# Kernel optimization log

Hardware: AMD Instinct MI355X
Metric: run time of the kernel (lower is better)

The kernel has to match this reference:

```python
import jax, jax.numpy as jnp
import numpy as np

E, N = 8192, 2048
D_EDGE, D_NODE, EMBED, HEADS = 64, 128, 32, 4


def setup_inputs() -> dict:
    key = jax.random.key(0)
    ks = jax.random.split(key, 12)
    s = 0.02
    edge_adj = jax.random.randint(ks[10], (E, E), 0, 2) > 0
    edge_adj = edge_adj | jnp.eye(E, dtype=bool)  # every edge attends to itself
    return {
        "edge_feats": jax.random.normal(ks[0], (E, D_EDGE), jnp.float32),
        "node_feats": jax.random.normal(ks[1], (N, D_NODE), jnp.float32),
        "Wn": s * jax.random.normal(ks[2], (D_NODE, D_EDGE), jnp.float32),
        "Wq": s * jax.random.normal(ks[3], (D_EDGE, D_EDGE), jnp.float32),
        "Wk": s * jax.random.normal(ks[4], (D_EDGE, D_EDGE), jnp.float32),
        "Wv": s * jax.random.normal(ks[5], (D_EDGE, D_EDGE), jnp.float32),
        "Wo": s * jax.random.normal(ks[6], (D_EDGE, D_EDGE), jnp.float32),
        "W1": s * jax.random.normal(ks[7], (D_EDGE, EMBED), jnp.float32),
        "b1": jnp.zeros((EMBED,), jnp.float32),
        "W2": s * jax.random.normal(ks[8], (EMBED, EMBED), jnp.float32),
        "b2": jnp.zeros((EMBED,), jnp.float32),
        "edge_index": jax.random.randint(ks[9], (2, E), 0, N, jnp.int32),
        "edge_adj": edge_adj,
    }


def reference(edge_feats, node_feats, Wn, Wq, Wk, Wv, Wo, W1, b1, W2, b2,
              edge_index, edge_adj):
    # --- EdgeAttention: enrich edges with endpoint node feats (irregular gather) ---
    src, dst = edge_index[0], edge_index[1]
    h = edge_feats + (node_feats[src] + node_feats[dst]) @ Wn  # [E, d_edge]
    hd = D_EDGE // HEADS
    q = (h @ Wq).reshape(E, HEADS, hd)
    k = (h @ Wk).reshape(E, HEADS, hd)
    v = (h @ Wv).reshape(E, HEADS, hd)
    scores = jnp.einsum("qhd,khd->hqk", q, k) / jnp.sqrt(jnp.float32(hd))
    scores = jnp.where(edge_adj[None, :, :], scores, jnp.float32(-1e9))
    attn = jax.nn.softmax(scores, axis=-1)                      # [H, E, E]
    ctx = jnp.einsum("hqk,khd->qhd", attn, v).reshape(E, D_EDGE)
    edge_out = ctx @ Wo                                          # [E, d_edge]
    # --- project: Linear -> GELU -> Linear ---
    x = jax.nn.gelu(edge_out @ W1 + b1)
    return x @ W2 + b2                                           # [E, embed_dim]
```

## Files before the change

kernel.cpp:

```cpp
#include <hip/hip_runtime.h>
#include <hip/hip_bf16.h>
#include <math.h>

#define E_N    8192
#define N_N    2048
#define D_EDGE 64
#define D_NODE 128
#define EMBED  32
#define HEADS  4
#define HD     16

typedef short bf16x8 __attribute__((ext_vector_type(8)));
typedef float f32x4  __attribute__((ext_vector_type(4)));
typedef float f32x16 __attribute__((ext_vector_type(16)));

__global__ __launch_bounds__(256) void prep_kernel(
    const float* __restrict__ edge_feats,
    const float* __restrict__ node_feats,
    const float* __restrict__ Wn,
    const float* __restrict__ Wq,
    const float* __restrict__ Wk,
    const float* __restrict__ Wv,
    const int*   __restrict__ edge_index,
    __hip_bfloat16* __restrict__ Qb,
    __hip_bfloat16* __restrict__ Kb,
    __hip_bfloat16* __restrict__ Vt,
    float* __restrict__ zero_base)
{
    {
        const int gtid = blockIdx.x * 256 + threadIdx.x;
        float4* z = (float4*)zero_base;
        const int nvec = (E_N * D_EDGE + E_N * HEADS) / 4;
        for (int i = gtid; i < nvec; i += 512 * 256)
            z[i] = make_float4(0.f, 0.f, 0.f, 0.f);
    }

    __shared__ float sL[4][D_NODE];
    __shared__ float hL[4][D_EDGE];
    const int lane = threadIdx.x & 63;
    const int es   = threadIdx.x >> 6;
    const int e_base = blockIdx.x * 16;

    for (int it = 0; it < 4; ++it) {
        const int e   = e_base + it * 4 + es;
        const int src = edge_index[e];
        const int dst = edge_index[E_N + e];

        sL[es][lane]      = node_feats[src * D_NODE + lane]
                          + node_feats[dst * D_NODE + lane];
        sL[es][lane + 64] = node_feats[src * D_NODE + 64 + lane]
                          + node_feats[dst * D_NODE + 64 + lane];
        __syncthreads();

        float h = edge_feats[e * D_EDGE + lane];
        #pragma unroll 16
        for (int i = 0; i < D_NODE; ++i)
            h = fmaf(sL[es][i], Wn[i * D_EDGE + lane], h);
        hL[es][lane] = h;
        __syncthreads();

        float q = 0.f, k = 0.f, v = 0.f;
        #pragma unroll 16
        for (int i = 0; i < D_EDGE; ++i) {
            const float hv = hL[es][i];
            q = fmaf(hv, Wq[i * D_EDGE + lane], q);
            k = fmaf(hv, Wk[i * D_EDGE + lane], k);
            v = fmaf(hv, Wv[i * D_EDGE + lane], v);
        }
        Qb[e * D_EDGE + lane] = __float2bfloat16(q * 0.25f);
        Kb[e * D_EDGE + lane] = __float2bfloat16(k);
        Vt[(size_t)lane * E_N + e] = __float2bfloat16(v);
        __syncthreads();
    }
}

__global__ __launch_bounds__(256) void attn_kernel(
    const __hip_bfloat16* __restrict__ Qb,
    const __hip_bfloat16* __restrict__ Kb,
    const __hip_bfloat16* __restrict__ Vt,
    const int* __restrict__ adj,
    float* __restrict__ O_acc,
    float* __restrict__ l_acc)
{
    __shared__ __hip_bfloat16 pS[4][32][40];

    const int tid  = threadIdx.x;
    const int wave = tid >> 6;
    const int lane = tid & 63;
    const int head = wave;
    const int qt = blockIdx.x >> 2;
    const int kq = blockIdx.x & 3;
    const int q0 = qt * 32;
    const int key_base = kq * 2048;
    const int col = lane & 31;

    const bf16x8 qf = *(const bf16x8*)(Qb + (size_t)(q0 + col) * D_EDGE
                                          + head * HD + ((lane >> 5) * 8));

    int moff[16];
    #pragma unroll
    for (int r = 0; r < 16; ++r) {
        const int row = (r & 3) + 8 * (r >> 2) + 4 * (lane >> 5);
        moff[r] = (q0 + row) * E_N + key_base + col;
    }

    const __hip_bfloat16* kptr = Kb + (size_t)(key_base + col) * D_EDGE
                                    + head * HD + ((lane >> 5) * 8);
    const __hip_bfloat16* vptr = Vt + (size_t)(head * HD + (lane & 15)) * E_N
                                    + key_base + ((lane >> 4) * 8);

    f32x4 acc0 = {0.f, 0.f, 0.f, 0.f};
    f32x4 acc1 = {0.f, 0.f, 0.f, 0.f};
    float l16[16];
    #pragma unroll
    for (int r = 0; r < 16; ++r) l16[r] = 0.f;

    __hip_bfloat16* pw = &pS[wave][4 * (lane >> 5)][col];
    const __hip_bfloat16* pA0 = &pS[wave][lane & 15][(lane >> 4) * 8];
    const __hip_bfloat16* pA1 = &pS[wave][16 + (lane & 15)][(lane >> 4) * 8];

    const f32x16 zero16 = {0.f,0.f,0.f,0.f, 0.f,0.f,0.f,0.f,
                           0.f,0.f,0.f,0.f, 0.f,0.f,0.f,0.f};

    for (int c = 0; c < 64; ++c) {
        int mw[16];
        #pragma unroll
        for (int r = 0; r < 16; ++r) mw[r] = adj[moff[r] + c * 32];

        const bf16x8 kf = *(const bf16x8*)(kptr + (size_t)c * 32 * D_EDGE);
        const bf16x8 vf = *(const bf16x8*)(vptr + c * 32);

        f32x16 S = __builtin_amdgcn_mfma_f32_32x32x16_bf16(qf, kf, zero16, 0, 0, 0);

        #pragma unroll
        for (int r = 0; r < 16; ++r) {
            const float p = mw[r] ? __expf(S[r]) : 0.f;
            l16[r] += p;
            pw[((r & 3) + 8 * (r >> 2)) * 40] = __float2bfloat16(p);
        }
        const bf16x8 a0 = *(const bf16x8*)pA0;
        const bf16x8 a1 = *(const bf16x8*)pA1;
        acc0 = __builtin_amdgcn_mfma_f32_16x16x32_bf16(a0, vf, acc0, 0, 0, 0);
        acc1 = __builtin_amdgcn_mfma_f32_16x16x32_bf16(a1, vf, acc1, 0, 0, 0);
    }

    #pragma unroll
    for (int r = 0; r < 16; ++r) {
        float s = l16[r];
        s += __shfl_xor(s, 1);  s += __shfl_xor(s, 2);  s += __shfl_xor(s, 4);
        s += __shfl_xor(s, 8);  s += __shfl_xor(s, 16);
        l16[r] = s;
    }
    if (col == 0) {
        #pragma unroll
        for (int r = 0; r < 16; ++r) {
            const int row = (r & 3) + 8 * (r >> 2) + 4 * (lane >> 5);
            atomicAdd(&l_acc[(q0 + row) * HEADS + head], l16[r]);
        }
    }

    #pragma unroll
    for (int r = 0; r < 4; ++r) {
        const int q  = (lane >> 4) * 4 + r;
        const int d  = head * HD + (lane & 15);
        atomicAdd(&O_acc[(size_t)(q0 + q) * D_EDGE + d],      acc0[r]);
        atomicAdd(&O_acc[(size_t)(q0 + 16 + q) * D_EDGE + d], acc1[r]);
    }
}

__global__ __launch_bounds__(256) void epilogue_kernel(
    const float* __restrict__ O_acc,
    const float* __restrict__ l_acc,
    const float* __restrict__ Wo,
    const float* __restrict__ W1,
    const float* __restrict__ b1,
    const float* __restrict__ W2,
    const float* __restrict__ b2,
    float* __restrict__ out)
{
    __shared__ float ctxS[16][D_EDGE];
    __shared__ float eoS[16][D_EDGE];
    __shared__ float xS[16][EMBED];
    const int tid = threadIdx.x;
    const int e0  = blockIdx.x * 16;

    {
        const int e = tid >> 4, d0 = (tid & 15) * 4;
        const float4 o = *(const float4*)(O_acc + (size_t)(e0 + e) * D_EDGE + d0);
        const float inv = 1.f / l_acc[(e0 + e) * HEADS + (d0 >> 4)];
        ctxS[e][d0]     = o.x * inv;
        ctxS[e][d0 + 1] = o.y * inv;
        ctxS[e][d0 + 2] = o.z * inv;
        ctxS[e][d0 + 3] = o.w * inv;
    }
    __syncthreads();

    for (int o = tid; o < 16 * D_EDGE; o += 256) {
        const int e = o >> 6, d = o & 63;
        float acc = 0.f;
        #pragma unroll 16
        for (int i = 0; i < D_EDGE; ++i)
            acc = fmaf(ctxS[e][i], Wo[i * D_EDGE + d], acc);
        eoS[e][d] = acc;
    }
    __syncthreads();

    for (int o = tid; o < 16 * EMBED; o += 256) {
        const int e = o >> 5, j = o & 31;
        float u = b1[j];
        #pragma unroll 16
        for (int i = 0; i < D_EDGE; ++i)
            u = fmaf(eoS[e][i], W1[i * EMBED + j], u);
        const float t = tanhf(0.7978845608028654f * (u + 0.044715f * u * u * u));
        xS[e][j] = 0.5f * u * (1.f + t);
    }
    __syncthreads();

    for (int o = tid; o < 16 * EMBED; o += 256) {
        const int e = o >> 5, j = o & 31;
        float v = b2[j];
        #pragma unroll
        for (int i = 0; i < EMBED; ++i)
            v = fmaf(xS[e][i], W2[i * EMBED + j], v);
        out[(size_t)(e0 + e) * EMBED + j] = v;
    }
}

extern "C" void kernel_launch(void* const* d_in, const int* in_sizes, int n_in,
                              void* d_out, int out_size, void* d_ws, size_t ws_size,
                              hipStream_t stream)
{
    (void)in_sizes; (void)n_in; (void)out_size; (void)ws_size;
    const float* edge_feats = (const float*)d_in[0];
    const float* node_feats = (const float*)d_in[1];
    const float* Wn = (const float*)d_in[2];
    const float* Wq = (const float*)d_in[3];
    const float* Wk = (const float*)d_in[4];
    const float* Wv = (const float*)d_in[5];
    const float* Wo = (const float*)d_in[6];
    const float* W1 = (const float*)d_in[7];
    const float* b1 = (const float*)d_in[8];
    const float* W2 = (const float*)d_in[9];
    const float* b2 = (const float*)d_in[10];
    const int*   edge_index = (const int*)d_in[11];
    const int*   adj = (const int*)d_in[12];

    __hip_bfloat16* Qb = (__hip_bfloat16*)d_ws;
    __hip_bfloat16* Kb = Qb + (size_t)E_N * D_EDGE;
    __hip_bfloat16* Vt = Kb + (size_t)E_N * D_EDGE;
    float* O_acc = (float*)(Vt + (size_t)E_N * D_EDGE);
    float* l_acc = O_acc + (size_t)E_N * D_EDGE;

    prep_kernel<<<E_N / 16, 256, 0, stream>>>(edge_feats, node_feats,
                                              Wn, Wq, Wk, Wv, edge_index,
                                              Qb, Kb, Vt, O_acc);
    attn_kernel<<<(E_N / 32) * 4, 256, 0, stream>>>(Qb, Kb, Vt, adj,
                                                    O_acc, l_acc);
    epilogue_kernel<<<E_N / 16, 256, 0, stream>>>(O_acc, l_acc,
                                                  Wo, W1, b1, W2, b2,
                                                  (float*)d_out);
}
```

Measured before the change: 524.0 us.

## Pack adjacency mask to bits once, transpose score MFMA, split keys eight ways

Adds a pre-pass that packs the int32 adjacency matrix into a bitmask, so the attention kernel reads 32x fewer mask bytes instead of re-reading the int mask once per head wave. The score MFMA now computes S transposed, which lets each lane own one query row: it writes probabilities as packed bf16 vectors and keeps a single row-sum, so the shuffle reductions go away. The key range is split into eight chunks instead of four, doubling the block count at the cost of more atomic traffic. The pack kernel still reads the full 256 MB int mask once, so total traffic only drops by the removed per-head re-reads.

```diff
diff --git a/kernel.cpp b/kernel.cpp
--- a/kernel.cpp
+++ b/kernel.cpp
@@ -9,6 +9,8 @@
 #define EMBED  32
 #define HEADS  4
 #define HD     16
+#define WPB    256
+#define PPAD   36
 
 typedef short bf16x8 __attribute__((ext_vector_type(8)));
 typedef float f32x4  __attribute__((ext_vector_type(4)));
@@ -74,95 +76,114 @@
     }
 }
 
+__global__ __launch_bounds__(256) void mask_pack_kernel(
+    const int* __restrict__ adj, unsigned int* __restrict__ adjb)
+{
+    const size_t t = (size_t)blockIdx.x * 256 + threadIdx.x;
+    const int4* src = (const int4*)(adj + t * 64);
+    unsigned int w0 = 0, w1 = 0;
+    #pragma unroll
+    for (int j = 0; j < 8; ++j) {
+        const int4 a = src[j];
+        w0 |= (unsigned)(a.x != 0) << (4 * j)
+            | (unsigned)(a.y != 0) << (4 * j + 1)
+            | (unsigned)(a.z != 0) << (4 * j + 2)
+            | (unsigned)(a.w != 0) << (4 * j + 3);
+    }
+    #pragma unroll
+    for (int j = 0; j < 8; ++j) {
+        const int4 a = src[8 + j];
+        w1 |= (unsigned)(a.x != 0) << (4 * j)
+            | (unsigned)(a.y != 0) << (4 * j + 1)
+            | (unsigned)(a.z != 0) << (4 * j + 2)
+            | (unsigned)(a.w != 0) << (4 * j + 3);
+    }
+    ((uint2*)adjb)[t] = make_uint2(w0, w1);
+}
+
 __global__ __launch_bounds__(256) void attn_kernel(
     const __hip_bfloat16* __restrict__ Qb,
     const __hip_bfloat16* __restrict__ Kb,
     const __hip_bfloat16* __restrict__ Vt,
-    const int* __restrict__ adj,
+    const unsigned int* __restrict__ adjb,
     float* __restrict__ O_acc,
     float* __restrict__ l_acc)
 {
-    __shared__ __hip_bfloat16 pS[4][32][40];
+    __shared__ __hip_bfloat16 pS[4][32][PPAD];
 
     const int tid  = threadIdx.x;
     const int wave = tid >> 6;
     const int lane = tid & 63;
     const int head = wave;
-    const int qt = blockIdx.x >> 2;
-    const int kq = blockIdx.x & 3;
+    const int qt = blockIdx.x >> 3;
+    const int kq = blockIdx.x & 7;
     const int q0 = qt * 32;
-    const int key_base = kq * 2048;
+    const int key_base = kq * 1024;
     const int col = lane & 31;
+    const int hh  = lane >> 5;
 
     const bf16x8 qf = *(const bf16x8*)(Qb + (size_t)(q0 + col) * D_EDGE
-                                          + head * HD + ((lane >> 5) * 8));
-
-    int moff[16];
-    #pragma unroll
-    for (int r = 0; r < 16; ++r) {
-        const int row = (r & 3) + 8 * (r >> 2) + 4 * (lane >> 5);
-        moff[r] = (q0 + row) * E_N + key_base + col;
-    }
-
+                                          + head * HD + hh * 8);
     const __hip_bfloat16* kptr = Kb + (size_t)(key_base + col) * D_EDGE
-                                    + head * HD + ((lane >> 5) * 8);
+                                    + head * HD + hh * 8;
     const __hip_bfloat16* vptr = Vt + (size_t)(head * HD + (lane & 15)) * E_N
                                     + key_base + ((lane >> 4) * 8);
+    const unsigned int* mrow = adjb + (size_t)(q0 + col) * WPB + kq * 32;
 
     f32x4 acc0 = {0.f, 0.f, 0.f, 0.f};
     f32x4 acc1 = {0.f, 0.f, 0.f, 0.f};
-    float l16[16];
-    #pragma unroll
-    for (int r = 0; r < 16; ++r) l16[r] = 0.f;
-
-    __hip_bfloat16* pw = &pS[wave][4 * (lane >> 5)][col];
+    float lp = 0.f;
+
+    __hip_bfloat16* pwr = &pS[wave][col][4 * hh];
     const __hip_bfloat16* pA0 = &pS[wave][lane & 15][(lane >> 4) * 8];
-    const __hip_bfloat16* pA1 = &pS[wave][16 + (lane & 15)][(lane >> 4) * 8];
-
-    const f32x16 zero16 = {0.f,0.f,0.f,0.f, 0.f,0.f,0.f,0.f,
-                           0.f,0.f,0.f,0.f, 0.f,0.f,0.f,0.f};
-
-    for (int c = 0; c < 64; ++c) {
-        int mw[16];
+    const __hip_bfloat16* pA1 = pA0 + 16 * PPAD;
+
+    const f32x16 z16 = {0.f,0.f,0.f,0.f, 0.f,0.f,0.f,0.f,
+                        0.f,0.f,0.f,0.f, 0.f,0.f,0.f,0.f};
+
+    for (int cw = 0; cw < 8; ++cw) {
+        const uint4 mv = *(const uint4*)(mrow + cw * 4);
         #pragma unroll
-        for (int r = 0; r < 16; ++r) mw[r] = adj[moff[r] + c * 32];
-
-        const bf16x8 kf = *(const bf16x8*)(kptr + (size_t)c * 32 * D_EDGE);
-        const bf16x8 vf = *(const bf16x8*)(vptr + c * 32);
-
-        f32x16 S = __builtin_amdgcn_mfma_f32_32x32x16_bf16(qf, kf, zero16, 0, 0, 0);
-
-        #pragma unroll
-        for (int r = 0; r < 16; ++r) {
-            const float p = mw[r] ? __expf(S[r]) : 0.f;
-            l16[r] += p;
-            pw[((r & 3) + 8 * (r >> 2)) * 40] = __float2bfloat16(p);
+        for (int cc = 0; cc < 4; ++cc) {
+            const int c = cw * 4 + cc;
+            const unsigned int w =
+                ((cc == 0) ? mv.x : (cc == 1) ? mv.y : (cc == 2) ? mv.z : mv.w)
+                >> (4 * hh);
+
+            const bf16x8 kf = *(const bf16x8*)(kptr + (size_t)c * 32 * D_EDGE);
+            const bf16x8 vf = *(const bf16x8*)(vptr + c * 32);
+
+            const f32x16 S = __builtin_amdgcn_mfma_f32_32x32x16_bf16(
+                                 kf, qf, z16, 0, 0, 0);
+
+            #pragma unroll
+            for (int g = 0; g < 4; ++g) {
+                const float p0 = ((w >> (8 * g + 0)) & 1u) ? __expf(S[4 * g + 0]) : 0.f;
+                const float p1 = ((w >> (8 * g + 1)) & 1u) ? __expf(S[4 * g + 1]) : 0.f;
+                const float p2 = ((w >> (8 * g + 2)) & 1u) ? __expf(S[4 * g + 2]) : 0.f;
+                const float p3 = ((w >> (8 * g + 3)) & 1u) ? __expf(S[4 * g + 3]) : 0.f;
+                lp += (p0 + p1) + (p2 + p3);
+                const __hip_bfloat162 lo = __float22bfloat162_rn(make_float2(p0, p1));
+                const __hip_bfloat162 hi = __float22bfloat162_rn(make_float2(p2, p3));
+                union { __hip_bfloat162 h2[2]; uint2 u; } cv;
+                cv.h2[0] = lo; cv.h2[1] = hi;
+                *(uint2*)(pwr + 8 * g) = cv.u;
+            }
+            const bf16x8 a0 = *(const bf16x8*)pA0;
+            const bf16x8 a1 = *(const bf16x8*)pA1;
+            acc0 = __builtin_amdgcn_mfma_f32_16x16x32_bf16(a0, vf, acc0, 0, 0, 0);
+            acc1 = __builtin_amdgcn_mfma_f32_16x16x32_bf16(a1, vf, acc1, 0, 0, 0);
         }
-        const bf16x8 a0 = *(const bf16x8*)pA0;
-        const bf16x8 a1 = *(const bf16x8*)pA1;
-        acc0 = __builtin_amdgcn_mfma_f32_16x16x32_bf16(a0, vf, acc0, 0, 0, 0);
-        acc1 = __builtin_amdgcn_mfma_f32_16x16x32_bf16(a1, vf, acc1, 0, 0, 0);
-    }
-
-    #pragma unroll
-    for (int r = 0; r < 16; ++r) {
-        float s = l16[r];
-        s += __shfl_xor(s, 1);  s += __shfl_xor(s, 2);  s += __shfl_xor(s, 4);
-        s += __shfl_xor(s, 8);  s += __shfl_xor(s, 16);
-        l16[r] = s;
-    }
-    if (col == 0) {
-        #pragma unroll
-        for (int r = 0; r < 16; ++r) {
-            const int row = (r & 3) + 8 * (r >> 2) + 4 * (lane >> 5);
-            atomicAdd(&l_acc[(q0 + row) * HEADS + head], l16[r]);
-        }
-    }
+    }
+
+    lp += __shfl_xor(lp, 32);
+    if (lane < 32)
+        atomicAdd(&l_acc[(q0 + col) * HEADS + head], lp);
 
     #pragma unroll
     for (int r = 0; r < 4; ++r) {
-        const int q  = (lane >> 4) * 4 + r;
-        const int d  = head * HD + (lane & 15);
+        const int q = (lane >> 4) * 4 + r;
+        const int d = head * HD + (lane & 15);
         atomicAdd(&O_acc[(size_t)(q0 + q) * D_EDGE + d],      acc0[r]);
         atomicAdd(&O_acc[(size_t)(q0 + 16 + q) * D_EDGE + d], acc1[r]);
     }
@@ -250,11 +271,13 @@
     __hip_bfloat16* Vt = Kb + (size_t)E_N * D_EDGE;
     float* O_acc = (float*)(Vt + (size_t)E_N * D_EDGE);
     float* l_acc = O_acc + (size_t)E_N * D_EDGE;
+    unsigned int* adjb = (unsigned int*)(l_acc + (size_t)E_N * HEADS);
 
     prep_kernel<<<E_N / 16, 256, 0, stream>>>(edge_feats, node_feats,
                                               Wn, Wq, Wk, Wv, edge_index,
                                               Qb, Kb, Vt, O_acc);
-    attn_kernel<<<(E_N / 32) * 4, 256, 0, stream>>>(Qb, Kb, Vt, adj,
+    mask_pack_kernel<<<(E_N / 64) * (E_N / 64) / 4, 256, 0, stream>>>(adj, adjb);
+    attn_kernel<<<(E_N / 32) * 8, 256, 0, stream>>>(Qb, Kb, Vt, adjb,
                                                     O_acc, l_acc);
     epilogue_kernel<<<E_N / 16, 256, 0, stream>>>(O_acc, l_acc,
                                                   Wo, W1, b1, W2, b2,
```

New measurement: 512.8 us. 2.1% less time.
